# Optimization experiments

Hardware: AMD Instinct MI355X
Metric: run time of the kernel (lower is better)

The kernel has to match this reference:

```python
import jax, jax.numpy as jnp
import numpy as np

N_QUBITS = 12
DEPTH = 4
OUT_DIM = 2
HID = 64
BATCH = 4096


def _u3(a, b, c):
    """Combined RZ(c) @ RY(b) @ RX(a) single-qubit gate, batched. a,b,c: [B] -> [B,2,2] complex."""
    ca, sa = jnp.cos(a / 2), jnp.sin(a / 2)
    cb, sb = jnp.cos(b / 2), jnp.sin(b / 2)
    RX = jnp.stack([jnp.stack([ca + 0j, -1j * sa], -1),
                    jnp.stack([-1j * sa, ca + 0j], -1)], -2)
    RY = jnp.stack([jnp.stack([cb + 0j, -sb + 0j], -1),
                    jnp.stack([sb + 0j, cb + 0j], -1)], -2)
    ez = jnp.exp(-1j * c / 2)
    zeros = jnp.zeros_like(ez)
    RZ = jnp.stack([jnp.stack([ez, zeros], -1),
                    jnp.stack([zeros, jnp.conj(ez)], -1)], -2)
    return jnp.einsum('bij,bjk,bkl->bil', RZ, RY, RX)


def _apply_1q(psi, U, q):
    """psi: [B]+[2]*n (wire 0 = most significant), U: [B,2,2]."""
    psi = jnp.moveaxis(psi, q + 1, 1)
    shp = psi.shape
    psi = psi.reshape(shp[0], 2, -1)
    psi = jnp.einsum('bij,bjr->bir', U, psi)
    return jnp.moveaxis(psi.reshape(shp), 1, q + 1)


def _apply_cnot(psi, c, t):
    """CNOT with control c, target t on psi [B]+[2]*n."""
    s0 = jax.lax.index_in_dim(psi, 0, axis=c + 1, keepdims=True)
    s1 = jax.lax.index_in_dim(psi, 1, axis=c + 1, keepdims=True)
    s1 = jnp.flip(s1, axis=t + 1)
    return jnp.concatenate([s0, s1], axis=c + 1)


def _circuit_expvals(params):
    """Batched hardware-efficient ansatz state-vector sim.
    params: [B, DEPTH, N_QUBITS, 3] -> PauliZ expvals [B, N_QUBITS]."""
    B = params.shape[0]
    n = N_QUBITS
    psi = jnp.zeros((B, 2 ** n), jnp.complex64).at[:, 0].set(1.0)
    psi = psi.reshape((B,) + (2,) * n)
    for l in range(DEPTH):
        for q in range(n):  # RX, RY, RZ per qubit (fused to one 2x2)
            U = _u3(params[:, l, q, 0], params[:, l, q, 1], params[:, l, q, 2])
            psi = _apply_1q(psi, U, q)
        for q in range(n):   # ring of CNOTs
            psi = _apply_cnot(psi, q, (q + 1) % n)
    probs = (psi.real ** 2 + psi.imag ** 2).reshape(B, 2 ** n)
    idx = jnp.arange(2 ** n)
    bits = (idx[None, :] >> (n - 1 - jnp.arange(n))[:, None]) & 1  # [n, 2^n]
    signs = (1.0 - 2.0 * bits).astype(jnp.float32)
    return probs @ signs.T  # <Z_q> = p(bit=0) - p(bit=1)


def setup_inputs() -> dict:
    key = jax.random.key(0)
    ks = jax.random.split(key, 5)
    n = N_QUBITS
    n_params = DEPTH * n * 3
    def w(k, shape):
        return (jax.random.normal(k, shape, jnp.float32) / np.sqrt(shape[0])).astype(jnp.float32)
    return {
        'noise': jax.random.normal(ks[0], (BATCH, n), jnp.float32),
        'W1': w(ks[1], (n, HID)), 'b1': jnp.zeros((HID,), jnp.float32),
        'W2': w(ks[2], (HID, n_params)), 'b2': jnp.zeros((n_params,), jnp.float32),
        'W3': w(ks[3], (n, HID)), 'b3': jnp.zeros((HID,), jnp.float32),
        'W4': w(ks[4], (HID, OUT_DIM)), 'b4': jnp.zeros((OUT_DIM,), jnp.float32),
    }


def reference(noise, W1, b1, W2, b2, W3, b3, W4, b4):
    h = jnp.tanh(noise @ W1 + b1)
    circ_params = (h @ W2 + b2).reshape(noise.shape[0], DEPTH, N_QUBITS, 3)
    meas = _circuit_expvals(circ_params)          # [B, n_qubits]
    h2 = jnp.tanh(meas @ W3 + b3)
    return h2 @ W4 + b4                            # [B, output_dim]
```

## Files before the change

kernel.cpp:

```cpp
#include <hip/hip_runtime.h>
#include <math.h>

#define NQ  12
#define TPB 256

typedef __attribute__((ext_vector_type(2))) float f2;


struct GF12 { unsigned row[12]; };

constexpr GF12 gf_id(){ GF12 m{}; for(int i=0;i<12;i++) m.row[i]=1u<<i; return m; }
constexpr GF12 gf_mul(const GF12&A,const GF12&B){
  GF12 r{};
  for(int i=0;i<12;i++){ unsigned acc=0;
    for(int k=0;k<12;k++) if((A.row[i]>>k)&1u) acc ^= B.row[k];
    r.row[i]=acc; }
  return r;
}
constexpr unsigned gf_apply(const GF12&A, unsigned x){
  unsigned y=0;
  for(int i=0;i<12;i++) y |= (unsigned)(__builtin_popcount(A.row[i]&x)&1)<<i;
  return y;
}
constexpr GF12 gf_cnot(int q){ GF12 m=gf_id(); int c=11-q, t=11-((q+1)%12); m.row[t]^=(1u<<c); return m; }
constexpr GF12 gf_inv(const GF12&A){
  unsigned a[12], inv[12];
  for(int i=0;i<12;i++){ a[i]=A.row[i]; inv[i]=1u<<i; }
  for(int c=0;c<12;c++){
    int p=-1;
    for(int r2=c;r2<12;r2++) if((a[r2]>>c)&1u){p=r2;break;}
    if(p<0) continue;
    unsigned ta=a[c]; a[c]=a[p]; a[p]=ta;
    unsigned ti=inv[c]; inv[c]=inv[p]; inv[p]=ti;
    for(int r2=0;r2<12;r2++) if(r2!=c && ((a[r2]>>c)&1u)){ a[r2]^=a[c]; inv[r2]^=inv[c]; }
  }
  GF12 R{}; for(int i=0;i<12;i++) R.row[i]=inv[i];
  return R;
}

struct Red { unsigned arr[12]; int hb[12]; int n; };
constexpr unsigned red_reduce(const Red& R, unsigned y){
  for(int i=0;i<R.n;i++) if((y>>R.hb[i])&1u) y ^= R.arr[i];
  return y;
}
constexpr bool red_add(Red& R, unsigned cand){
  unsigned y = red_reduce(R, cand);
  if(!y) return false;
  int h=0;
  for(int b2=11;b2>=1;b2--) if((y>>b2)&1u){ h=b2; break; }
  R.arr[R.n]=y; R.hb[R.n]=h; R.n++;
  return true;
}

struct PairT {
  unsigned M0[4], M1[4];
  unsigned sz[16], gx[16];
  unsigned rB[8], roff[16];
};
struct AllT { PairT pr[6]; unsigned mq[12], uq[12]; bool ok; };

constexpr AllT makeAll(){
  AllT T{}; T.ok=true;
  GF12 D=gf_id(); for(int q=0;q<12;q++) D=gf_mul(gf_cnot(q),D);
  GF12 Cm=gf_id(); for(int q=11;q>=0;q--) Cm=gf_mul(gf_cnot(q),Cm);
  unsigned V[12][4]{},R[12][4]{},rfin[12]{};
  GF12 Mm=gf_id(), Mi=gf_id();
  for(int l=0;l<4;l++){
    for(int q=0;q<12;q++){
      int b=11-q; unsigned v=0;
      for(int j=0;j<12;j++) v|=((Mi.row[j]>>b)&1u)<<j;
      V[l*3+q/4][q&3]=v; R[l*3+q/4][q&3]=Mm.row[b];
    }
    Mm=gf_mul(D,Mm); Mi=gf_mul(Cm,Mi);
  }
  for(int q=0;q<12;q++) rfin[q]=Mm.row[11-q];

  GF12 Sg=gf_id(); Sg.row[1]|=1u<<4; Sg.row[2]|=1u<<5; Sg.row[3]|=1u<<6;

  GF12 Tprev{}, Tprev_inv{};
  for(int m=0;m<6;m++){
    const int p0=2*m, p1=p0+1;
    for(int pp=p0;pp<=p1;pp++) for(int j=0;j<4;j++) for(int i=0;i<4;i++){
      int par=__builtin_popcount(R[pp][j]&V[pp][i])&1;
      if(par!=((i==j)?1:0)) T.ok=false;
    }
    Red S{};
    for(int i=0;i<4;i++){ red_add(S,V[p0][i]); red_add(S,V[p1][i]); }
    for(unsigned x=1;x<4096 && S.n<10;x++) red_add(S,x);
    if(S.n!=10) T.ok=false;
    Red S12=S, RA{}, RB{};
    for(int i=0;i<4;i++){ red_add(RA,V[p0][i]); red_add(RB,V[p1][i]); }
    unsigned B[8]{};
    Red resR{};
    for(int k=0;k<6;k++){
      unsigned pick=0;
      if(m>0){
        unsigned res=(k<4)?(1u<<k):0u;
        for(unsigned hi=(k<4)?0u:1u; hi<256 && !pick; hi++){
          unsigned y=res|(hi<<4);
          unsigned x=gf_apply(Tprev_inv,y);
          if(red_reduce(S,x)) continue;
          if(!red_reduce(RA,x)) continue;
          if(!red_reduce(RB,x)) continue;
          pick=x;
        }
        for(unsigned y=1;y<4096 && !pick;y++){
          unsigned x=gf_apply(Tprev_inv,y);
          if(red_reduce(S,x)) continue;
          if(!red_reduce(RA,x)) continue;
          if(!red_reduce(RB,x)) continue;
          if(k<4){ unsigned rb=y&15u; if(!rb || !red_reduce(resR,rb)) continue; }
          pick=x;
        }
      }
      if(!pick){
        for(unsigned x=1;x<4096 && !pick;x++){
          if(red_reduce(S,x)) continue;
          if(!red_reduce(RA,x)) continue;
          if(!red_reduce(RB,x)) continue;
          pick=x;
        }
      }
      if(!pick){ T.ok=false; pick=1; }
      if(m>0 && k<4){ unsigned rb=gf_apply(Tprev,pick)&15u; if(rb) red_add(resR,rb); }
      red_add(RA,pick); red_add(RB,pick);
      B[k]=pick;
    }
    for(int k=6;k<8;k++){
      unsigned pick=0;
      for(unsigned x=1;x<4096 && !pick;x++) if(red_reduce(S12,x)) pick=x;
      if(!pick){ T.ok=false; pick=1; }
      red_add(S12,pick); B[k]=pick;
    }
    if(S12.n!=12) T.ok=false;
    GF12 Z{};
    for(int i=0;i<12;i++){
      unsigned rr=0;
      for(int k=0;k<4;k++) rr |= ((V[p1][k]>>i)&1u)<<k;
      for(int k=0;k<8;k++) rr |= ((B[k]>>i)&1u)<<(4+k);
      Z.row[i]=rr;
    }
    GF12 Tp=gf_inv(Z);
    { GF12 I2=gf_mul(Tp,Z); for(int i=0;i<12;i++) if(I2.row[i]!=(1u<<i)) T.ok=false; }
    for(int j=0;j<4;j++){
      unsigned m0=0,m1=0;
      for(int k=0;k<8;k++){
        m0 |= (unsigned)(__builtin_popcount(R[p0][j]&B[k])&1)<<k;
        m1 |= (unsigned)(__builtin_popcount(R[p1][j]&B[k])&1)<<k;
      }
      T.pr[m].M0[j]=m0; T.pr[m].M1[j]=m1;
    }
    unsigned zeta[4]{}, gam[4]{};
    for(int i=0;i<4;i++){
      unsigned d=gf_apply(Tp,V[p0][i]);
      if(d>>10) T.ok=false;
      zeta[i]=d&15u; gam[i]=(d>>4)&63u;
    }
    unsigned zmap[16]{}; bool seen[16]{};
    for(int z=0;z<16;z++){
      unsigned zz=0;
      for(int i=0;i<4;i++) if((z>>i)&1) zz^=zeta[i];
      zmap[z]=zz;
      if(seen[zz]) T.ok=false; seen[zz]=true;
    }
    for(int zp=0;zp<16;zp++){
      unsigned src=0;
      for(int z=0;z<16;z++) if(zmap[z]==(unsigned)zp) src=(unsigned)z;
      unsigned gg=0;
      for(int i=0;i<4;i++) if((src>>i)&1) gg^=gam[i];
      T.pr[m].sz[zp]=src; T.pr[m].gx[zp]=gg;
    }
    for(int z=0;z<16;z++){
      unsigned c0=0,c1=0,gg=0,bb=0;
      for(int i=0;i<4;i++){
        if((z>>i)&1){ c0^=V[p0][i]; gg^=gam[i]; }
        if((zmap[z]>>i)&1) c1^=V[p1][i];
      }
      for(int k=0;k<6;k++) if((gg>>k)&1) bb^=B[k];
      if((c0^c1^bb)!=0) T.ok=false;
    }
    if(m>0){
      for(int k=0;k<8;k++) T.pr[m].rB[k]=gf_apply(Tprev,B[k]);
      for(int z=0;z<16;z++){
        unsigned c=0;
        for(int i=0;i<4;i++) if((z>>i)&1) c^=V[p0][i];
        T.pr[m].roff[z]=gf_apply(Tprev,c);
      }
    }
    GF12 Tnew=gf_mul(Sg,Tp), Tnew_inv=gf_mul(Z,Sg);
    { GF12 I2=gf_mul(Tnew,Tnew_inv); for(int i=0;i<12;i++) if(I2.row[i]!=(1u<<i)) T.ok=false; }
    Tprev=Tnew; Tprev_inv=Tnew_inv;
    if(m==5){
      for(int q=0;q<12;q++){
        unsigned u=0,mm=0;
        for(int i=0;i<4;i++) u |= (unsigned)(__builtin_popcount(rfin[q]&V[11][i])&1)<<i;
        for(int k=0;k<8;k++) mm |= (unsigned)(__builtin_popcount(rfin[q]&B[k])&1)<<k;
        T.uq[q]=u; T.mq[q]=mm;
      }
    }
  }
  return T;
}

constexpr AllT hA = makeAll();
static_assert(hA.ok, "GF(2) paired-bpermute table self-check failed");

#define GATE_PK(SS,MM,JJ) do { \
    const int _lb = pl + 4*(JJ); \
    const unsigned _sg = ((unsigned)(__popc((MM) & (unsigned)t) & 1)) << 31; \
    const float _ar = __uint_as_float((unsigned)__builtin_amdgcn_readlane((int)cur, _lb+0)); \
    const float _ai = __uint_as_float(((unsigned)__builtin_amdgcn_readlane((int)cur, _lb+1)) ^ _sg); \
    const float _br = __uint_as_float(((unsigned)__builtin_amdgcn_readlane((int)cur, _lb+2)) ^ _sg); \
    const float _bi = __uint_as_float((unsigned)__builtin_amdgcn_readlane((int)cur, _lb+3)); \
    const f2 A0 = {_ar,_ar}, A1 = {-_ai,_ai}, B0 = {_br,_br}, B1 = {-_bi,_bi}; \
    _Pragma("unroll") \
    for (int s0=0; s0<16; ++s0){ \
      if ((s0 >> (JJ)) & 1) continue; \
      const int s1 = s0 | (1<<(JJ)); \
      const f2 X = SS[s0], Y = SS[s1]; \
      const f2 Xs = __builtin_shufflevector(X,X,1,0); \
      const f2 Ys = __builtin_shufflevector(Y,Y,1,0); \
      SS[s0] = __builtin_elementwise_fma(A0,X, \
               __builtin_elementwise_fma(A1,Xs, \
               __builtin_elementwise_fma(B0,Y, B1*Ys))); \
      SS[s1] = __builtin_elementwise_fma(A0,Y, \
               __builtin_elementwise_fma(-A1,Ys, \
               __builtin_elementwise_fma(-B0,X, B1*Xs))); \
    } \
  } while(0)

template<int M>
__device__ __forceinline__ void do_pair(f2 S[16], f2 Sn[16],
                                        unsigned c0, unsigned c1, unsigned c2,
                                        unsigned t, float2* s2, float4* s4)
{
  constexpr PairT P = hA.pr[M];
  if constexpr (M > 0){
    unsigned base=0;
    #pragma unroll
    for(int k=0;k<8;++k) base ^= ((t>>k)&1u) ? P.rB[k] : 0u;
    #pragma unroll
    for(int z=0;z<16;++z){ float2 v=s2[base ^ P.roff[z]]; S[z].x=v.x; S[z].y=v.y; }
  }
  { constexpr int ci=(2*M)>>2;
    const unsigned cur=(ci==0)?c0:((ci==1)?c1:c2);
    const int pl=((2*M)&3)<<4;
    GATE_PK(S,P.M0[0],0); GATE_PK(S,P.M0[1],1); GATE_PK(S,P.M0[2],2); GATE_PK(S,P.M0[3],3); }
  { const unsigned t4=t<<2;
    #pragma unroll
    for(int zp=0; zp<16; ++zp){
      const int idx=(int)(t4 ^ (P.gx[zp]<<2));
      Sn[zp].x=__uint_as_float((unsigned)__builtin_amdgcn_ds_bpermute(idx,(int)__float_as_uint(S[P.sz[zp]].x)));
      Sn[zp].y=__uint_as_float((unsigned)__builtin_amdgcn_ds_bpermute(idx,(int)__float_as_uint(S[P.sz[zp]].y)));
    } }
  { constexpr int ci=(2*M+1)>>2;
    const unsigned cur=(ci==0)?c0:((ci==1)?c1:c2);
    const int pl=((2*M+1)&3)<<4;
    GATE_PK(Sn,P.M1[0],0); GATE_PK(Sn,P.M1[1],1); GATE_PK(Sn,P.M1[2],2); GATE_PK(Sn,P.M1[3],3); }
  if constexpr (M < 5){
    __syncthreads();
    const unsigned wb=t<<3;
    #pragma unroll
    for(int k=0;k<8;++k)
      s4[wb | ((unsigned)k ^ (t&7u))] =
        make_float4(Sn[2*k].x, Sn[2*k].y, Sn[2*k+1].x, Sn[2*k+1].y);
    __syncthreads();
  }
}

__global__ void __launch_bounds__(TPB, 5)
qgen(const float* __restrict__ noise,
     const float* __restrict__ W1, const float* __restrict__ b1,
     const float* __restrict__ W2, const float* __restrict__ b2,
     const float* __restrict__ W3, const float* __restrict__ b3,
     const float* __restrict__ W4, const float* __restrict__ b4,
     float* __restrict__ out)
{
  __shared__ float2 s2[4096];
  float*  sf=(float*)s2;
  float4* s4=(float4*)s2;

  const unsigned t = threadIdx.x;
  const int b = blockIdx.x;
  const int lane = t & 63;

  if (t < 12) sf[400+t] = noise[b*12+t];
  __syncthreads();
  if (t < 64){
    float a = b1[t];
    #pragma unroll
    for (int k=0;k<12;++k) a = fmaf(sf[400+k], W1[k*64+t], a);
    sf[192+t] = tanhf(a);
  }
  __syncthreads();
  if (t < 144){
    float a = b2[t];
    #pragma unroll 16
    for (int j=0;j<64;++j) a = fmaf(sf[192+j], W2[j*144+t], a);
    sf[256+t] = a;
  }
  __syncthreads();
  if (t < 48){
    float aa = sf[256+3*t+0]*0.5f, bb = sf[256+3*t+1]*0.5f, c = sf[256+3*t+2]*0.5f;
    float sa,ca,sb,cb,sc2,cc;
    __sincosf(aa,&sa,&ca); __sincosf(bb,&sb,&cb); __sincosf(c,&sc2,&cc);
    float A=cb*ca, B=sb*sa, Cc=sb*ca, Dd=cb*sa;
    s4[t] = make_float4(fmaf(cc,A,  sc2*B),  fmaf(cc,B, -sc2*A),
                        fmaf(-cc,Cc,-sc2*Dd), fmaf(sc2,Cc,-cc*Dd));
  }
  __syncthreads();
  const unsigned* su=(const unsigned*)s2;
  const unsigned cu0=su[lane], cu1=su[64+lane], cu2=su[128+lane];
  __syncthreads();

  f2 S[16], Sn[16];
  #pragma unroll
  for(int k=0;k<16;++k){ S[k].x=0.f; S[k].y=0.f; }
  if(t==0) S[0].x=1.0f;

  do_pair<0>(S,Sn,cu0,cu1,cu2,t,s2,s4);
  do_pair<1>(S,Sn,cu0,cu1,cu2,t,s2,s4);
  do_pair<2>(S,Sn,cu0,cu1,cu2,t,s2,s4);
  do_pair<3>(S,Sn,cu0,cu1,cu2,t,s2,s4);
  do_pair<4>(S,Sn,cu0,cu1,cu2,t,s2,s4);
  do_pair<5>(S,Sn,cu0,cu1,cu2,t,s2,s4);

  float H[16];
  #pragma unroll
  for(int z=0;z<16;++z) H[z]=fmaf(Sn[z].x,Sn[z].x, Sn[z].y*Sn[z].y);
  #pragma unroll
  for(int st=1;st<16;st<<=1){
    #pragma unroll
    for(int z=0;z<16;++z){
      if(z & st) continue;
      float a0=H[z], a1=H[z|st];
      H[z]=a0+a1; H[z|st]=a0-a1;
    }
  }
  float acc[12];
  #pragma unroll
  for(int q=0;q<12;++q){
    const unsigned ls=((unsigned)(__popc(hA.mq[q]&t)&1))<<31;
    acc[q]=__uint_as_float(__float_as_uint(H[hA.uq[q]])^ls);
  }

  __syncthreads();
  const int wv=t>>6;
  #pragma unroll
  for(int q=0;q<12;++q){
    float v=acc[q];
    #pragma unroll
    for(int off=32;off>0;off>>=1) v += __shfl_down(v,off,64);
    if(lane==0) sf[wv*12+q]=v;
  }
  __syncthreads();
  if(t<12) sf[64+t]=sf[t]+sf[12+t]+sf[24+t]+sf[36+t];
  __syncthreads();

  if(t<64){
    float a=b3[t];
    #pragma unroll
    for(int k=0;k<12;++k) a=fmaf(sf[64+k],W3[k*64+t],a);
    float h2=tanhf(a);
    float p0=h2*W4[2*t+0], p1=h2*W4[2*t+1];
    #pragma unroll
    for(int off=32;off>0;off>>=1){ p0+=__shfl_down(p0,off,64); p1+=__shfl_down(p1,off,64); }
    if(t==0){ out[2*b+0]=p0+b4[0]; out[2*b+1]=p1+b4[1]; }
  }
}

extern "C" void kernel_launch(void* const* d_in, const int* in_sizes, int n_in,
                              void* d_out, int out_size, void* d_ws, size_t ws_size,
                              hipStream_t stream)
{
  const float* noise=(const float*)d_in[0];
  const float* W1=(const float*)d_in[1];
  const float* b1=(const float*)d_in[2];
  const float* W2=(const float*)d_in[3];
  const float* b2=(const float*)d_in[4];
  const float* W3=(const float*)d_in[5];
  const float* b3=(const float*)d_in[6];
  const float* W4=(const float*)d_in[7];
  const float* b4=(const float*)d_in[8];
  float* out=(float*)d_out;
  const int batch=in_sizes[0]/NQ;
  qgen<<<batch,TPB,0,stream>>>(noise,W1,b1,W2,b2,W3,b3,W4,b4,out);
}
```

Before: 201.2 us.

## Halve shared state buffer by exchanging real and imaginary parts in two passes

The shared-memory state exchange between gate pairs now moves the real parts and the imaginary parts in two separate passes through a 16 KB buffer, where it used to move full complex values through a 32 KB buffer. The smaller LDS footprint lets more blocks fit per CU, and the launch bound is raised from 5 to 8 blocks to match. The cost is twice as many barriers and LDS round trips per boundary, and the tighter register budget may cause spills.

After: 276.4 us. +37.4%, slower.

```diff
diff --git a/kernel.cpp b/kernel.cpp
--- a/kernel.cpp
+++ b/kernel.cpp
@@ -232,16 +232,9 @@
 template<int M>
 __device__ __forceinline__ void do_pair(f2 S[16], f2 Sn[16],
                                         unsigned c0, unsigned c1, unsigned c2,
-                                        unsigned t, float2* s2, float4* s4)
+                                        unsigned t)
 {
   constexpr PairT P = hA.pr[M];
-  if constexpr (M > 0){
-    unsigned base=0;
-    #pragma unroll
-    for(int k=0;k<8;++k) base ^= ((t>>k)&1u) ? P.rB[k] : 0u;
-    #pragma unroll
-    for(int z=0;z<16;++z){ float2 v=s2[base ^ P.roff[z]]; S[z].x=v.x; S[z].y=v.y; }
-  }
   { constexpr int ci=(2*M)>>2;
     const unsigned cur=(ci==0)?c0:((ci==1)?c1:c2);
     const int pl=((2*M)&3)<<4;
@@ -257,18 +250,34 @@
     const unsigned cur=(ci==0)?c0:((ci==1)?c1:c2);
     const int pl=((2*M+1)&3)<<4;
     GATE_PK(Sn,P.M1[0],0); GATE_PK(Sn,P.M1[1],1); GATE_PK(Sn,P.M1[2],2); GATE_PK(Sn,P.M1[3],3); }
-  if constexpr (M < 5){
-    __syncthreads();
-    const unsigned wb=t<<3;
-    #pragma unroll
-    for(int k=0;k<8;++k)
-      s4[wb | ((unsigned)k ^ (t&7u))] =
-        make_float4(Sn[2*k].x, Sn[2*k].y, Sn[2*k+1].x, Sn[2*k+1].y);
-    __syncthreads();
-  }
-}
-
-__global__ void __launch_bounds__(TPB, 5)
+}
+
+template<int M>
+__device__ __forceinline__ void boundary(const f2 Sn[16], f2 S[16], unsigned t,
+                                         float* sfx, float2* sfx2)
+{
+  constexpr PairT P = hA.pr[M+1];
+  unsigned base=0;
+  #pragma unroll
+  for(int k=0;k<8;++k) base ^= ((t>>k)&1u) ? P.rB[k] : 0u;
+  const unsigned wb = t<<3;
+  __syncthreads();
+  #pragma unroll
+  for(int k=0;k<8;++k)
+    sfx2[wb | ((unsigned)k ^ (t&7u))] = make_float2(Sn[2*k].x, Sn[2*k+1].x);
+  __syncthreads();
+  #pragma unroll
+  for(int z=0;z<16;++z) S[z].x = sfx[base ^ P.roff[z]];
+  __syncthreads();
+  #pragma unroll
+  for(int k=0;k<8;++k)
+    sfx2[wb | ((unsigned)k ^ (t&7u))] = make_float2(Sn[2*k].y, Sn[2*k+1].y);
+  __syncthreads();
+  #pragma unroll
+  for(int z=0;z<16;++z) S[z].y = sfx[base ^ P.roff[z]];
+}
+
+__global__ void __launch_bounds__(TPB, 8)
 qgen(const float* __restrict__ noise,
      const float* __restrict__ W1, const float* __restrict__ b1,
      const float* __restrict__ W2, const float* __restrict__ b2,
@@ -276,9 +285,10 @@
      const float* __restrict__ W4, const float* __restrict__ b4,
      float* __restrict__ out)
 {
-  __shared__ float2 s2[4096];
-  float*  sf=(float*)s2;
-  float4* s4=(float4*)s2;
+  __shared__ float4 sbuf[1024];
+  float*  sf=(float*)sbuf;
+  float2* s2=(float2*)sbuf;
+  float4* s4=(float4*)sbuf;
 
   const unsigned t = threadIdx.x;
   const int b = blockIdx.x;
@@ -309,7 +319,7 @@
                         fmaf(-cc,Cc,-sc2*Dd), fmaf(sc2,Cc,-cc*Dd));
   }
   __syncthreads();
-  const unsigned* su=(const unsigned*)s2;
+  const unsigned* su=(const unsigned*)sbuf;
   const unsigned cu0=su[lane], cu1=su[64+lane], cu2=su[128+lane];
   __syncthreads();
 
@@ -318,12 +328,17 @@
   for(int k=0;k<16;++k){ S[k].x=0.f; S[k].y=0.f; }
   if(t==0) S[0].x=1.0f;
 
-  do_pair<0>(S,Sn,cu0,cu1,cu2,t,s2,s4);
-  do_pair<1>(S,Sn,cu0,cu1,cu2,t,s2,s4);
-  do_pair<2>(S,Sn,cu0,cu1,cu2,t,s2,s4);
-  do_pair<3>(S,Sn,cu0,cu1,cu2,t,s2,s4);
-  do_pair<4>(S,Sn,cu0,cu1,cu2,t,s2,s4);
-  do_pair<5>(S,Sn,cu0,cu1,cu2,t,s2,s4);
+  do_pair<0>(S,Sn,cu0,cu1,cu2,t);
+  boundary<0>(Sn,S,t,sf,s2);
+  do_pair<1>(S,Sn,cu0,cu1,cu2,t);
+  boundary<1>(Sn,S,t,sf,s2);
+  do_pair<2>(S,Sn,cu0,cu1,cu2,t);
+  boundary<2>(Sn,S,t,sf,s2);
+  do_pair<3>(S,Sn,cu0,cu1,cu2,t);
+  boundary<3>(Sn,S,t,sf,s2);
+  do_pair<4>(S,Sn,cu0,cu1,cu2,t);
+  boundary<4>(Sn,S,t,sf,s2);
+  do_pair<5>(S,Sn,cu0,cu1,cu2,t);
 
   float H[16];
   #pragma unroll
```

## Process two batch elements per block, interleaving their state exchanges

Applied to the files above, without the earlier changes.

Each block now simulates two batch samples, so the grid is halved. The gate computation of one sample is interleaved with the shared-memory read and write of the other, through one shared buffer. The goal is to hide LDS exchange latency and barrier stalls behind independent arithmetic. In exchange each thread keeps more registers live, so the launch-bounds occupancy hint drops from 5 to 4 blocks, and an even batch size is assumed.

After: 201.2 us. About the same (+0.0%).

```diff
diff --git a/kernel.cpp b/kernel.cpp
--- a/kernel.cpp
+++ b/kernel.cpp
@@ -232,16 +232,9 @@
 template<int M>
 __device__ __forceinline__ void do_pair(f2 S[16], f2 Sn[16],
                                         unsigned c0, unsigned c1, unsigned c2,
-                                        unsigned t, float2* s2, float4* s4)
+                                        unsigned t)
 {
   constexpr PairT P = hA.pr[M];
-  if constexpr (M > 0){
-    unsigned base=0;
-    #pragma unroll
-    for(int k=0;k<8;++k) base ^= ((t>>k)&1u) ? P.rB[k] : 0u;
-    #pragma unroll
-    for(int z=0;z<16;++z){ float2 v=s2[base ^ P.roff[z]]; S[z].x=v.x; S[z].y=v.y; }
-  }
   { constexpr int ci=(2*M)>>2;
     const unsigned cur=(ci==0)?c0:((ci==1)?c1:c2);
     const int pl=((2*M)&3)<<4;
@@ -257,18 +250,57 @@
     const unsigned cur=(ci==0)?c0:((ci==1)?c1:c2);
     const int pl=((2*M+1)&3)<<4;
     GATE_PK(Sn,P.M1[0],0); GATE_PK(Sn,P.M1[1],1); GATE_PK(Sn,P.M1[2],2); GATE_PK(Sn,P.M1[3],3); }
-  if constexpr (M < 5){
-    __syncthreads();
-    const unsigned wb=t<<3;
-    #pragma unroll
-    for(int k=0;k<8;++k)
-      s4[wb | ((unsigned)k ^ (t&7u))] =
-        make_float4(Sn[2*k].x, Sn[2*k].y, Sn[2*k+1].x, Sn[2*k+1].y);
-    __syncthreads();
-  }
-}
-
-__global__ void __launch_bounds__(TPB, 5)
+}
+
+__device__ __forceinline__ void writeS(const f2 Sn[16], float4* s4, unsigned t)
+{
+  const unsigned wb = t<<3;
+  #pragma unroll
+  for(int k=0;k<8;++k)
+    s4[wb | ((unsigned)k ^ (t&7u))] =
+      make_float4(Sn[2*k].x, Sn[2*k].y, Sn[2*k+1].x, Sn[2*k+1].y);
+}
+
+template<int MP>
+__device__ __forceinline__ void readS(f2 S[16], const float2* s2, unsigned t)
+{
+  constexpr PairT P = hA.pr[MP];
+  unsigned base=0;
+  #pragma unroll
+  for(int k=0;k<8;++k) base ^= ((t>>k)&1u) ? P.rB[k] : 0u;
+  #pragma unroll
+  for(int z=0;z<16;++z){ float2 v=s2[base ^ P.roff[z]]; S[z].x=v.x; S[z].y=v.y; }
+}
+
+__device__ __forceinline__ void initS(f2 S[16], unsigned t)
+{
+  #pragma unroll
+  for(int k=0;k<16;++k){ S[k].x=0.f; S[k].y=0.f; }
+  if(t==0) S[0].x=1.0f;
+}
+
+__device__ __forceinline__ void measure(const f2 Sn[16], float acc[12], unsigned t)
+{
+  float H[16];
+  #pragma unroll
+  for(int z=0;z<16;++z) H[z]=fmaf(Sn[z].x,Sn[z].x, Sn[z].y*Sn[z].y);
+  #pragma unroll
+  for(int st=1;st<16;st<<=1){
+    #pragma unroll
+    for(int z=0;z<16;++z){
+      if(z & st) continue;
+      float a0=H[z], a1=H[z|st];
+      H[z]=a0+a1; H[z|st]=a0-a1;
+    }
+  }
+  #pragma unroll
+  for(int q=0;q<12;++q){
+    const unsigned ls=((unsigned)(__popc(hA.mq[q]&t)&1))<<31;
+    acc[q]=__uint_as_float(__float_as_uint(H[hA.uq[q]])^ls);
+  }
+}
+
+__global__ void __launch_bounds__(TPB, 4)
 qgen(const float* __restrict__ noise,
      const float* __restrict__ W1, const float* __restrict__ b1,
      const float* __restrict__ W2, const float* __restrict__ b2,
@@ -276,85 +308,96 @@
      const float* __restrict__ W4, const float* __restrict__ b4,
      float* __restrict__ out)
 {
-  __shared__ float2 s2[4096];
-  float*  sf=(float*)s2;
-  float4* s4=(float4*)s2;
+  __shared__ float2 sbuf[4096];
+  float*  sf=(float*)sbuf;
+  float2* s2=(float2*)sbuf;
+  float4* s4=(float4*)sbuf;
 
   const unsigned t = threadIdx.x;
   const int b = blockIdx.x;
   const int lane = t & 63;
 
-  if (t < 12) sf[400+t] = noise[b*12+t];
-  __syncthreads();
-  if (t < 64){
-    float a = b1[t];
-    #pragma unroll
-    for (int k=0;k<12;++k) a = fmaf(sf[400+k], W1[k*64+t], a);
-    sf[192+t] = tanhf(a);
-  }
-  __syncthreads();
-  if (t < 144){
-    float a = b2[t];
-    #pragma unroll 16
-    for (int j=0;j<64;++j) a = fmaf(sf[192+j], W2[j*144+t], a);
-    sf[256+t] = a;
-  }
-  __syncthreads();
-  if (t < 48){
-    float aa = sf[256+3*t+0]*0.5f, bb = sf[256+3*t+1]*0.5f, c = sf[256+3*t+2]*0.5f;
-    float sa,ca,sb,cb,sc2,cc;
-    __sincosf(aa,&sa,&ca); __sincosf(bb,&sb,&cb); __sincosf(c,&sc2,&cc);
-    float A=cb*ca, B=sb*sa, Cc=sb*ca, Dd=cb*sa;
-    s4[t] = make_float4(fmaf(cc,A,  sc2*B),  fmaf(cc,B, -sc2*A),
-                        fmaf(-cc,Cc,-sc2*Dd), fmaf(sc2,Cc,-cc*Dd));
-  }
-  __syncthreads();
-  const unsigned* su=(const unsigned*)s2;
-  const unsigned cu0=su[lane], cu1=su[64+lane], cu2=su[128+lane];
+  #pragma unroll
+  for(int e=0;e<2;++e){
+    if (t < 12) sf[448+t] = noise[(2*b+e)*12+t];
+    __syncthreads();
+    if (t < 64){
+      float a = b1[t];
+      #pragma unroll
+      for (int k=0;k<12;++k) a = fmaf(sf[448+k], W1[k*64+t], a);
+      sf[464+t] = tanhf(a);
+    }
+    __syncthreads();
+    if (t < 144){
+      float a = b2[t];
+      #pragma unroll 16
+      for (int j=0;j<64;++j) a = fmaf(sf[464+j], W2[j*144+t], a);
+      sf[544+t] = a;
+    }
+    __syncthreads();
+    if (t < 48){
+      float aa = sf[544+3*t+0]*0.5f, bb = sf[544+3*t+1]*0.5f, c = sf[544+3*t+2]*0.5f;
+      float sa,ca,sb,cb,sc2,cc;
+      __sincosf(aa,&sa,&ca); __sincosf(bb,&sb,&cb); __sincosf(c,&sc2,&cc);
+      float A=cb*ca, B=sb*sa, Cc=sb*ca, Dd=cb*sa;
+      s4[e*48+t] = make_float4(fmaf(cc,A,  sc2*B),  fmaf(cc,B, -sc2*A),
+                               fmaf(-cc,Cc,-sc2*Dd), fmaf(sc2,Cc,-cc*Dd));
+    }
+    __syncthreads();
+  }
+  const unsigned* su=(const unsigned*)sbuf;
+  const unsigned cA0=su[lane],     cA1=su[64+lane],  cA2=su[128+lane];
+  const unsigned cB0=su[192+lane], cB1=su[256+lane], cB2=su[320+lane];
   __syncthreads();
 
   f2 S[16], Sn[16];
-  #pragma unroll
-  for(int k=0;k<16;++k){ S[k].x=0.f; S[k].y=0.f; }
-  if(t==0) S[0].x=1.0f;
-
-  do_pair<0>(S,Sn,cu0,cu1,cu2,t,s2,s4);
-  do_pair<1>(S,Sn,cu0,cu1,cu2,t,s2,s4);
-  do_pair<2>(S,Sn,cu0,cu1,cu2,t,s2,s4);
-  do_pair<3>(S,Sn,cu0,cu1,cu2,t,s2,s4);
-  do_pair<4>(S,Sn,cu0,cu1,cu2,t,s2,s4);
-  do_pair<5>(S,Sn,cu0,cu1,cu2,t,s2,s4);
-
-  float H[16];
-  #pragma unroll
-  for(int z=0;z<16;++z) H[z]=fmaf(Sn[z].x,Sn[z].x, Sn[z].y*Sn[z].y);
-  #pragma unroll
-  for(int st=1;st<16;st<<=1){
-    #pragma unroll
-    for(int z=0;z<16;++z){
-      if(z & st) continue;
-      float a0=H[z], a1=H[z|st];
-      H[z]=a0+a1; H[z|st]=a0-a1;
-    }
-  }
-  float acc[12];
+
+  initS(S,t);
+  do_pair<0>(S,Sn,cA0,cA1,cA2,t);
+  writeS(Sn,s4,t);
+  __syncthreads();
+  initS(S,t);
+  do_pair<0>(S,Sn,cB0,cB1,cB2,t);
+  readS<1>(S,s2,t);
+  __syncthreads();
+  writeS(Sn,s4,t);
+  __syncthreads();
+
+  do_pair<1>(S,Sn,cA0,cA1,cA2,t); readS<1>(S,s2,t); __syncthreads(); writeS(Sn,s4,t); __syncthreads();
+  do_pair<1>(S,Sn,cB0,cB1,cB2,t); readS<2>(S,s2,t); __syncthreads(); writeS(Sn,s4,t); __syncthreads();
+  do_pair<2>(S,Sn,cA0,cA1,cA2,t); readS<2>(S,s2,t); __syncthreads(); writeS(Sn,s4,t); __syncthreads();
+  do_pair<2>(S,Sn,cB0,cB1,cB2,t); readS<3>(S,s2,t); __syncthreads(); writeS(Sn,s4,t); __syncthreads();
+  do_pair<3>(S,Sn,cA0,cA1,cA2,t); readS<3>(S,s2,t); __syncthreads(); writeS(Sn,s4,t); __syncthreads();
+  do_pair<3>(S,Sn,cB0,cB1,cB2,t); readS<4>(S,s2,t); __syncthreads(); writeS(Sn,s4,t); __syncthreads();
+  do_pair<4>(S,Sn,cA0,cA1,cA2,t); readS<4>(S,s2,t); __syncthreads(); writeS(Sn,s4,t); __syncthreads();
+  do_pair<4>(S,Sn,cB0,cB1,cB2,t); readS<5>(S,s2,t); __syncthreads(); writeS(Sn,s4,t); __syncthreads();
+
+  do_pair<5>(S,Sn,cA0,cA1,cA2,t);
+  float accA[12]; measure(Sn,accA,t);
+  readS<5>(S,s2,t);
+  do_pair<5>(S,Sn,cB0,cB1,cB2,t);
+  float accB[12]; measure(Sn,accB,t);
+
+  __syncthreads();
+
+  const int wv=t>>6;
   #pragma unroll
   for(int q=0;q<12;++q){
-    const unsigned ls=((unsigned)(__popc(hA.mq[q]&t)&1))<<31;
-    acc[q]=__uint_as_float(__float_as_uint(H[hA.uq[q]])^ls);
-  }
-
-  __syncthreads();
-  const int wv=t>>6;
-  #pragma unroll
-  for(int q=0;q<12;++q){
-    float v=acc[q];
+    float v=accA[q];
     #pragma unroll
     for(int off=32;off>0;off>>=1) v += __shfl_down(v,off,64);
     if(lane==0) sf[wv*12+q]=v;
   }
-  __syncthreads();
-  if(t<12) sf[64+t]=sf[t]+sf[12+t]+sf[24+t]+sf[36+t];
+  #pragma unroll
+  for(int q=0;q<12;++q){
+    float v=accB[q];
+    #pragma unroll
+    for(int off=32;off>0;off>>=1) v += __shfl_down(v,off,64);
+    if(lane==0) sf[100+wv*12+q]=v;
+  }
+  __syncthreads();
+  if(t<12)            sf[64+t]      = sf[t]        +sf[12+t]      +sf[24+t]      +sf[36+t];
+  else if(t>=64&&t<76) sf[164+(t-64)]= sf[100+(t-64)]+sf[112+(t-64)]+sf[124+(t-64)]+sf[136+(t-64)];
   __syncthreads();
 
   if(t<64){
@@ -365,7 +408,17 @@
     float p0=h2*W4[2*t+0], p1=h2*W4[2*t+1];
     #pragma unroll
     for(int off=32;off>0;off>>=1){ p0+=__shfl_down(p0,off,64); p1+=__shfl_down(p1,off,64); }
-    if(t==0){ out[2*b+0]=p0+b4[0]; out[2*b+1]=p1+b4[1]; }
+    if(lane==0){ out[4*b+0]=p0+b4[0]; out[4*b+1]=p1+b4[1]; }
+  } else if(t<128){
+    const int t2=t-64;
+    float a=b3[t2];
+    #pragma unroll
+    for(int k=0;k<12;++k) a=fmaf(sf[164+k],W3[k*64+t2],a);
+    float h2=tanhf(a);
+    float p0=h2*W4[2*t2+0], p1=h2*W4[2*t2+1];
+    #pragma unroll
+    for(int off=32;off>0;off>>=1){ p0+=__shfl_down(p0,off,64); p1+=__shfl_down(p1,off,64); }
+    if(lane==0){ out[4*b+2]=p0+b4[0]; out[4*b+3]=p1+b4[1]; }
   }
 }
 
@@ -384,5 +437,5 @@
   const float* b4=(const float*)d_in[8];
   float* out=(float*)d_out;
   const int batch=in_sizes[0]/NQ;
-  qgen<<<batch,TPB,0,stream>>>(noise,W1,b1,W2,b2,W3,b3,W4,b4,out);
-}
+  qgen<<<batch/2,TPB,0,stream>>>(noise,W1,b1,W2,b2,W3,b3,W4,b4,out);
+}
```
